# Kernel optimization log

Hardware: AMD Instinct MI355X
Metric: run time of the kernel (lower is better)

The kernel has to match this reference:

```python
import jax, jax.numpy as jnp
import numpy as np

N = 100000      # nodes
E = 1600000     # edges per direction
G = 512         # graphs in the batch
NEG_SLOPE = 0.2 # PyG GATConv default


def _gat_conv(x, W, a_s, a_d, b, src, dst, n):
    # PyG GATConv, heads=1: h = x W; e_ij = LeakyReLU(a_s.h_j + a_d.h_i);
    # softmax over incoming edges of i; out_i = sum_j alpha_ij h_j + b
    h = x @ W                                   # [N, F]
    al_s = h @ a_s                              # [N]
    al_d = h @ a_d                              # [N]
    e = jax.nn.leaky_relu(al_s[src] + al_d[dst], NEG_SLOPE)   # [E+N]
    m = jax.ops.segment_max(e, dst, num_segments=n)
    ex = jnp.exp(e - m[dst])
    denom = jax.ops.segment_sum(ex, dst, num_segments=n)
    coef = ex / denom[dst]                      # softmax per destination
    out = jax.ops.segment_sum(h[src] * coef[:, None], dst, num_segments=n)
    return out + b


def _branch(x, edge_index, W1, as1, ad1, b1, W2, as2, ad2, b2, batch, n, g):
    # add self loops (GATConv default add_self_loops=True)
    loops = jnp.arange(n)
    src = jnp.concatenate([edge_index[0], loops])
    dst = jnp.concatenate([edge_index[1], loops])
    h = jax.nn.relu(_gat_conv(x, W1, as1, ad1, b1, src, dst, n))
    # dropout is identity at eval time
    h = jax.nn.relu(_gat_conv(h, W2, as2, ad2, b2, src, dst, n))
    s = jax.ops.segment_sum(h, batch, num_segments=g)
    cnt = jax.ops.segment_sum(jnp.ones((n,), h.dtype), batch, num_segments=g)
    return s / jnp.maximum(cnt, 1.0)[:, None]    # scatter_mean


def setup_inputs() -> dict:
    key = jax.random.key(0)
    ks = jax.random.split(key, 24)
    d_in, d_hid, d_out, n_cls = 128, 128, 128, 4
    x = jax.random.normal(ks[0], (N, d_in), jnp.float32)
    td = jax.random.randint(ks[1], (2, E), 0, N)
    bu = jax.random.randint(ks[2], (2, E), 0, N)
    batch = jnp.sort(jax.random.randint(ks[3], (N,), 0, G))

    def lin(k, shape):
        return jax.random.normal(k, shape, jnp.float32) * (1.0 / np.sqrt(shape[0]))

    inp = {"x": x, "td_edge_index": td, "bu_edge_index": bu, "batch": batch}
    i = 4
    for br in ("td", "bu"):
        for layer, (di, do) in (("1", (d_in, d_hid)), ("2", (d_hid, d_out))):
            inp[f"{br}_W{layer}"] = lin(ks[i], (di, do)); i += 1
            inp[f"{br}_as{layer}"] = lin(ks[i], (do,)); i += 1
            inp[f"{br}_ad{layer}"] = lin(ks[i], (do,)); i += 1
            inp[f"{br}_b{layer}"] = jnp.zeros((do,), jnp.float32)
    inp["fc_W"] = lin(ks[i], (2 * d_out, n_cls)); i += 1
    inp["fc_b"] = jnp.zeros((n_cls,), jnp.float32)
    return inp


def reference(x, td_edge_index, bu_edge_index, batch,
              td_W1, td_as1, td_ad1, td_b1, td_W2, td_as2, td_ad2, td_b2,
              bu_W1, bu_as1, bu_ad1, bu_b1, bu_W2, bu_as2, bu_ad2, bu_b2,
              fc_W, fc_b):
    td = _branch(x, td_edge_index, td_W1, td_as1, td_ad1, td_b1,
                 td_W2, td_as2, td_ad2, td_b2, batch, N, G)
    bu = _branch(x, bu_edge_index, bu_W1, bu_as1, bu_ad1, bu_b1,
                 bu_W2, bu_as2, bu_ad2, bu_b2, batch, N, G)
    out = jnp.concatenate([bu, td], axis=1) @ fc_W + fc_b   # [G, num_class]
    return jax.nn.log_softmax(out, axis=1)
```

## Files before the change

kernel.cpp:

```cpp
#include <hip/hip_runtime.h>

#define FD 128
#define SB 512
#define CHK 8192

typedef __attribute__((ext_vector_type(8))) short bf16x8;
typedef __attribute__((ext_vector_type(4))) float f32x4;

static inline size_t roundup256(size_t x) { return (x + 255) & ~(size_t)255; }

__device__ __forceinline__ unsigned short f2bf(float f) {
    unsigned u = __float_as_uint(f);
    u += 0x7FFFu + ((u >> 16) & 1u);
    return (unsigned short)(u >> 16);
}
__device__ __forceinline__ float bflo(unsigned v) { return __uint_as_float(v << 16); }
__device__ __forceinline__ float bfhi(unsigned v) { return __uint_as_float(v & 0xFFFF0000u); }

__global__ __launch_bounds__(256) void wprep_kernel(
    const float* __restrict__ w0, const float* __restrict__ w1,
    const float* __restrict__ w2, const float* __restrict__ w3,
    unsigned short* __restrict__ out)
{
    const int widx = blockIdx.x >> 6;
    const float* src = (widx == 0) ? w0 : (widx == 1) ? w1 : (widx == 2) ? w2 : w3;
    const int flat = (blockIdx.x & 63) * 256 + threadIdx.x;
    const int k = flat >> 7, n = flat & 127;
    const int dest = ((((n >> 4) * 4 + (k >> 5)) * 4 + ((k >> 3) & 3)) * 16 + (n & 15)) * 8 + (k & 7);
    out[widx * 16384 + dest] = f2bf(src[flat]);
}

__global__ __launch_bounds__(256) void bucket_count_kernel(
    const int* __restrict__ td_ei, const int* __restrict__ bu_ei,
    int* __restrict__ table, int E, int NB, int NBLK)
{
    __shared__ int cnt[512];
    const int blk = blockIdx.x;
    const int br = blk / NBLK, c = blk % NBLK;
    const int* edst = (br ? bu_ei : td_ei) + E;
    for (int i = threadIdx.x; i < NB; i += 256) cnt[i] = 0;
    __syncthreads();
    const int k0 = c * CHK;
    #pragma unroll 4
    for (int j = 0; j < CHK / 256; ++j) {
        const int k = k0 + j * 256 + threadIdx.x;
        if (k < E) atomicAdd(&cnt[((unsigned)edst[k]) >> 8], 1);
    }
    __syncthreads();
    for (int i = threadIdx.x; i < NB; i += 256)
        table[(br * NB + i) * NBLK + c] = cnt[i];
}

__global__ __launch_bounds__(256) void bucket_scatter_kernel(
    const int* __restrict__ td_ei, const int* __restrict__ bu_ei,
    const int* __restrict__ scanned, int* __restrict__ bucketed,
    int E, int NB, int NBLK)
{
    __shared__ int cur[512];
    const int blk = blockIdx.x;
    const int br = blk / NBLK, c = blk % NBLK;
    const int* ei = br ? bu_ei : td_ei;
    for (int i = threadIdx.x; i < NB; i += 256)
        cur[i] = scanned[(br * NB + i) * NBLK + c];
    __syncthreads();
    const int k0 = c * CHK;
    #pragma unroll 4
    for (int j = 0; j < CHK / 256; ++j) {
        const int k = k0 + j * 256 + threadIdx.x;
        if (k < E) {
            const int d = ei[E + k], s = ei[k];
            const int pos = atomicAdd(&cur[((unsigned)d) >> 8], 1);
            bucketed[pos] = ((d & 255) << 24) | s;
        }
    }
}

__global__ __launch_bounds__(256) void bucket_finalize_kernel(
    const int* __restrict__ scanned, const int* __restrict__ bucketed,
    int* __restrict__ esorted, int* __restrict__ rowptr,
    int E, int N, int NB, int NBLK)
{
    __shared__ int bins[256], off[256], curs[256], tmp[256];
    const int gb = blockIdx.x;
    const int br = gb / NB, lb = gb % NB;
    const int tid = threadIdx.x;
    const int base = scanned[gb * NBLK];
    const int next = scanned[(gb + 1) * NBLK];
    const int s = next - base;

    bins[tid] = 0;
    __syncthreads();
    for (int i = base + tid; i < base + s; i += 256)
        atomicAdd(&bins[((unsigned)bucketed[i]) >> 24], 1);
    __syncthreads();
    const int v = bins[tid];
    tmp[tid] = v;
    __syncthreads();
    for (int o = 1; o < 256; o <<= 1) {
        const int t = (tid >= o) ? tmp[tid - o] : 0;
        __syncthreads();
        tmp[tid] += t;
        __syncthreads();
    }
    off[tid] = tmp[tid] - v;
    curs[tid] = tmp[tid] - v;
    const int nd = N - lb * 256;
    if (tid < nd && tid < 256) rowptr[br * N + lb * 256 + tid] = base + off[tid];
    if (gb == 2 * NB - 1 && tid == 0) rowptr[2 * N] = 2 * E;
    __syncthreads();
    for (int i = base + tid; i < base + s; i += 256) {
        const int p = bucketed[i];
        const int r = atomicAdd(&curs[((unsigned)p) >> 24], 1);
        esorted[base + r] = br * N + (p & 0xFFFFFF);
    }
}

__global__ __launch_bounds__(SB) void scan_block_kernel(
    const int* __restrict__ in, int* __restrict__ out, int* __restrict__ bsum, int n)
{
    __shared__ int sh[SB];
    const int tid = threadIdx.x;
    const int i = blockIdx.x * SB + tid;
    int v = (i < n) ? in[i] : 0;
    sh[tid] = v;
    __syncthreads();
    for (int off = 1; off < SB; off <<= 1) {
        int t = (tid >= off) ? sh[tid - off] : 0;
        __syncthreads();
        sh[tid] += t;
        __syncthreads();
    }
    if (i < n) out[i] = sh[tid] - v;
    if (tid == SB - 1) bsum[blockIdx.x] = sh[tid];
}

__global__ __launch_bounds__(SB) void scan_top_kernel(int* __restrict__ bsum, int nb)
{
    __shared__ int sh[SB];
    const int tid = threadIdx.x;
    int v = (tid < nb) ? bsum[tid] : 0;
    sh[tid] = v;
    __syncthreads();
    for (int off = 1; off < SB; off <<= 1) {
        int t = (tid >= off) ? sh[tid - off] : 0;
        __syncthreads();
        sh[tid] += t;
        __syncthreads();
    }
    if (tid < nb) bsum[tid] = sh[tid] - v;
}

__global__ __launch_bounds__(SB) void scan_add_kernel(
    int* __restrict__ arr, const int* __restrict__ bsum, int n, int total)
{
    int i = blockIdx.x * SB + threadIdx.x;
    if (i < n) arr[i] += bsum[blockIdx.x];
    if (i == 0) arr[n] = total;
}

template<bool A_F32>
__global__ __launch_bounds__(256) void gemm_mfma_kernel(
    const float* __restrict__ Xf, const unsigned short* __restrict__ Xb,
    const unsigned short* __restrict__ Wfrag,
    const float* __restrict__ as0, const float* __restrict__ ad0,
    const float* __restrict__ as1, const float* __restrict__ ad1,
    unsigned short* __restrict__ H16, float* __restrict__ als, float* __restrict__ ald,
    int nrows, int xbstride)
{
    const int tid = threadIdx.x;
    const int br  = blockIdx.y;
    const int w = tid >> 6, l = tid & 63, lg = l >> 4, cl = l & 15;
    const int lr0 = blockIdx.x * 64 + w * 16;
    const int lr  = lr0 + cl;
    const unsigned short* Wb = Wfrag + br * 16384;
    const float* a_s = br ? as1 : as0;
    const float* a_d = br ? ad1 : ad0;

    bf16x8 a[4];
    if (lr < nrows) {
        if (A_F32) {
            const float* xp = Xf + (size_t)(br * xbstride + lr) * FD + lg * 8;
            #pragma unroll
            for (int ks = 0; ks < 4; ++ks) {
                const float4 v0 = *(const float4*)(xp + ks * 32);
                const float4 v1 = *(const float4*)(xp + ks * 32 + 4);
                bf16x8 t;
                t[0] = (short)f2bf(v0.x); t[1] = (short)f2bf(v0.y);
                t[2] = (short)f2bf(v0.z); t[3] = (short)f2bf(v0.w);
                t[4] = (short)f2bf(v1.x); t[5] = (short)f2bf(v1.y);
                t[6] = (short)f2bf(v1.z); t[7] = (short)f2bf(v1.w);
                a[ks] = t;
            }
        } else {
            const unsigned short* xp = Xb + (size_t)(br * xbstride + lr) * FD + lg * 8;
            #pragma unroll
            for (int ks = 0; ks < 4; ++ks) a[ks] = *(const bf16x8*)(xp + ks * 32);
        }
    } else {
        #pragma unroll
        for (int ks = 0; ks < 4; ++ks)
            #pragma unroll
            for (int j = 0; j < 8; ++j) a[ks][j] = 0;
    }

    f32x4 acc[8];
    #pragma unroll
    for (int t = 0; t < 8; ++t)
        #pragma unroll
        for (int j = 0; j < 4; ++j) acc[t][j] = 0.f;

    #pragma unroll
    for (int t = 0; t < 8; ++t) {
        #pragma unroll
        for (int ks = 0; ks < 4; ++ks) {
            const bf16x8 b = *(const bf16x8*)&Wb[(((t * 4 + ks) * 4 + lg) * 16 + cl) * 8];
            acc[t] = __builtin_amdgcn_mfma_f32_16x16x32_bf16(a[ks], b, acc[t], 0, 0, 0);
        }
    }

    float asv[8], adv[8];
    #pragma unroll
    for (int t = 0; t < 8; ++t) { asv[t] = a_s[t * 16 + cl]; adv[t] = a_d[t * 16 + cl]; }

    #pragma unroll
    for (int jj = 0; jj < 4; ++jj) {
        const int lrow = lr0 + 4 * lg + jj;
        float ps = 0.f, pd = 0.f;
        #pragma unroll
        for (int t = 0; t < 8; ++t) {
            ps = fmaf(acc[t][jj], asv[t], ps);
            pd = fmaf(acc[t][jj], adv[t], pd);
        }
        #pragma unroll
        for (int off = 8; off; off >>= 1) {
            ps += __shfl_down(ps, off, 16);
            pd += __shfl_down(pd, off, 16);
        }
        if (lrow < nrows) {
            const size_t grow = (size_t)br * nrows + lrow;
            #pragma unroll
            for (int t = 0; t < 8; ++t)
                H16[grow * FD + t * 16 + cl] = f2bf(acc[t][jj]);
            if (cl == 0) { als[grow] = ps; ald[grow] = pd; }
        }
    }
}

__global__ __launch_bounds__(256) void gat_aggregate_kernel(
    const int* __restrict__ rowptr, const int* __restrict__ esorted,
    const float* __restrict__ als, const float* __restrict__ ald,
    const unsigned short* __restrict__ H16,
    const float* __restrict__ b0, const float* __restrict__ b1,
    unsigned short* __restrict__ out16, int n2, int N)
{
    const int d    = (int)((blockIdx.x * 256u + threadIdx.x) >> 5);
    const int lane = threadIdx.x & 31;
    if (d >= n2) return;
    const int start = rowptr[d], end = rowptr[d + 1];
    const int deg = end - start;
    const float ald_d = ald[d];
    const int c = lane * 4;
    const float* bias = (d < N) ? b0 : b1;

    const uint2 hs = *(const uint2*)&H16[(size_t)d * FD + c];

    float e_self = als[d] + ald_d;
    e_self = fmaxf(e_self, 0.2f * e_self);

    float e_reg = -INFINITY;
    int src_reg = 0;
    if (lane < deg) {
        src_reg = esorted[start + lane];
        float t = als[src_reg] + ald_d;
        e_reg = fmaxf(t, 0.2f * t);
    }
    float m = e_reg;
    for (int j = start + 32 + lane; j < end; j += 32) {
        float t = als[esorted[j]] + ald_d;
        m = fmaxf(m, fmaxf(t, 0.2f * t));
    }
    #pragma unroll
    for (int off = 16; off; off >>= 1) m = fmaxf(m, __shfl_xor(m, off, 32));
    m = fmaxf(m, e_self);

    const float w_self = __expf(e_self - m);
    const float w_reg  = __expf(e_reg - m);

    float dsum = w_reg;
    #pragma unroll
    for (int off = 16; off; off >>= 1) dsum += __shfl_xor(dsum, off, 32);
    float denom = dsum + w_self;

    float a0 = w_self * bflo(hs.x);
    float a1 = w_self * bfhi(hs.x);
    float a2 = w_self * bflo(hs.y);
    float a3 = w_self * bfhi(hs.y);

    const int dmin = deg < 32 ? deg : 32;
    int j = 0;
    for (; j + 7 < dmin; j += 8) {
        uint2 hv[8];
        float w[8];
        #pragma unroll
        for (int q = 0; q < 8; ++q) {
            const int s = __shfl(src_reg, j + q, 32);
            w[q] = __shfl(w_reg, j + q, 32);
            hv[q] = *(const uint2*)&H16[(size_t)s * FD + c];
        }
        #pragma unroll
        for (int q = 0; q < 8; ++q) {
            a0 = fmaf(w[q], bflo(hv[q].x), a0);
            a1 = fmaf(w[q], bfhi(hv[q].x), a1);
            a2 = fmaf(w[q], bflo(hv[q].y), a2);
            a3 = fmaf(w[q], bfhi(hv[q].y), a3);
        }
    }
    for (; j < dmin; ++j) {
        const int   s = __shfl(src_reg, j, 32);
        const float w = __shfl(w_reg, j, 32);
        const uint2 hv = *(const uint2*)&H16[(size_t)s * FD + c];
        a0 = fmaf(w, bflo(hv.x), a0);
        a1 = fmaf(w, bfhi(hv.x), a1);
        a2 = fmaf(w, bflo(hv.y), a2);
        a3 = fmaf(w, bfhi(hv.y), a3);
    }
    for (int jj = 32; jj < deg; ++jj) {
        const int s = esorted[start + jj];
        float t = als[s] + ald_d;
        t = fmaxf(t, 0.2f * t);
        const float w = __expf(t - m);
        denom += w;
        const uint2 hv = *(const uint2*)&H16[(size_t)s * FD + c];
        a0 = fmaf(w, bflo(hv.x), a0);
        a1 = fmaf(w, bfhi(hv.x), a1);
        a2 = fmaf(w, bflo(hv.y), a2);
        a3 = fmaf(w, bfhi(hv.y), a3);
    }
    const float inv = 1.f / denom;
    const float4 bb = *(const float4*)&bias[c];
    const float o0 = fmaxf(fmaf(a0, inv, bb.x), 0.f);
    const float o1 = fmaxf(fmaf(a1, inv, bb.y), 0.f);
    const float o2 = fmaxf(fmaf(a2, inv, bb.z), 0.f);
    const float o3 = fmaxf(fmaf(a3, inv, bb.w), 0.f);
    uint2 ov;
    ov.x = (unsigned)f2bf(o0) | ((unsigned)f2bf(o1) << 16);
    ov.y = (unsigned)f2bf(o2) | ((unsigned)f2bf(o3) << 16);
    *(uint2*)&out16[(size_t)d * FD + c] = ov;
}

__global__ __launch_bounds__(256) void pool_mean_kernel(
    const unsigned short* __restrict__ Hb, const int* __restrict__ batch,
    float* __restrict__ pooled_td, float* __restrict__ pooled_bu, int n)
{
    __shared__ float sh[3][FD];
    const int g = blockIdx.x;
    const int br = blockIdx.y;
    int lo = 0, hi = n;
    while (lo < hi) { int mid = (lo + hi) >> 1; if (batch[mid] < g) lo = mid + 1; else hi = mid; }
    int start = lo;
    hi = n;
    while (lo < hi) { int mid = (lo + hi) >> 1; if (batch[mid] < g + 1) lo = mid + 1; else hi = mid; }
    int end = lo;
    const int cp = threadIdx.x & 63;
    const int q  = threadIdx.x >> 6;
    const size_t rbase = (size_t)br * n;
    float ax = 0.f, ay = 0.f;
    for (int i = start + q; i < end; i += 4) {
        unsigned v = ((const unsigned*)Hb)[(rbase + i) * 64 + cp];
        ax += bflo(v);
        ay += bfhi(v);
    }
    if (q) { sh[q - 1][cp * 2] = ax; sh[q - 1][cp * 2 + 1] = ay; }
    __syncthreads();
    if (!q) {
        float tx = ax + sh[0][cp * 2] + sh[1][cp * 2] + sh[2][cp * 2];
        float ty = ay + sh[0][cp * 2 + 1] + sh[1][cp * 2 + 1] + sh[2][cp * 2 + 1];
        float inv = 1.f / fmaxf((float)(end - start), 1.f);
        float* out = br ? pooled_bu : pooled_td;
        out[(size_t)g * FD + cp * 2]     = tx * inv;
        out[(size_t)g * FD + cp * 2 + 1] = ty * inv;
    }
}

__global__ __launch_bounds__(256) void fc_logsoftmax_kernel(
    const float* __restrict__ bu, const float* __restrict__ td,
    const float* __restrict__ Wf, const float* __restrict__ bf,
    float* __restrict__ out, int g)
{
    const int wid  = (int)((blockIdx.x * 256u + threadIdx.x) >> 6);
    const int lane = threadIdx.x & 63;
    if (wid >= g) return;
    const float f0 = bu[(size_t)wid * FD + lane];
    const float f1 = bu[(size_t)wid * FD + 64 + lane];
    const float f2 = td[(size_t)wid * FD + lane];
    const float f3 = td[(size_t)wid * FD + 64 + lane];
    const float4 w0 = *(const float4*)&Wf[lane * 4];
    const float4 w1 = *(const float4*)&Wf[(64 + lane) * 4];
    const float4 w2 = *(const float4*)&Wf[(128 + lane) * 4];
    const float4 w3 = *(const float4*)&Wf[(192 + lane) * 4];
    float l0 = f0 * w0.x + f1 * w1.x + f2 * w2.x + f3 * w3.x;
    float l1 = f0 * w0.y + f1 * w1.y + f2 * w2.y + f3 * w3.y;
    float l2 = f0 * w0.z + f1 * w1.z + f2 * w2.z + f3 * w3.z;
    float l3 = f0 * w0.w + f1 * w1.w + f2 * w2.w + f3 * w3.w;
    #pragma unroll
    for (int off = 32; off; off >>= 1) {
        l0 += __shfl_xor(l0, off, 64);
        l1 += __shfl_xor(l1, off, 64);
        l2 += __shfl_xor(l2, off, 64);
        l3 += __shfl_xor(l3, off, 64);
    }
    if (lane == 0) {
        l0 += bf[0]; l1 += bf[1]; l2 += bf[2]; l3 += bf[3];
        float m = fmaxf(fmaxf(l0, l1), fmaxf(l2, l3));
        float ssum = expf(l0 - m) + expf(l1 - m) + expf(l2 - m) + expf(l3 - m);
        float ls = logf(ssum);
        out[(size_t)wid * 4 + 0] = l0 - m - ls;
        out[(size_t)wid * 4 + 1] = l1 - m - ls;
        out[(size_t)wid * 4 + 2] = l2 - m - ls;
        out[(size_t)wid * 4 + 3] = l3 - m - ls;
    }
}

extern "C" void kernel_launch(void* const* d_in, const int* in_sizes, int n_in,
                              void* d_out, int out_size, void* d_ws, size_t ws_size,
                              hipStream_t stream)
{
    const float* x      = (const float*)d_in[0];
    const int*   td_ei  = (const int*)d_in[1];
    const int*   bu_ei  = (const int*)d_in[2];
    const int*   batch  = (const int*)d_in[3];
    const float* td_W1  = (const float*)d_in[4];
    const float* td_as1 = (const float*)d_in[5];
    const float* td_ad1 = (const float*)d_in[6];
    const float* td_b1  = (const float*)d_in[7];
    const float* td_W2  = (const float*)d_in[8];
    const float* td_as2 = (const float*)d_in[9];
    const float* td_ad2 = (const float*)d_in[10];
    const float* td_b2  = (const float*)d_in[11];
    const float* bu_W1  = (const float*)d_in[12];
    const float* bu_as1 = (const float*)d_in[13];
    const float* bu_ad1 = (const float*)d_in[14];
    const float* bu_b1  = (const float*)d_in[15];
    const float* bu_W2  = (const float*)d_in[16];
    const float* bu_as2 = (const float*)d_in[17];
    const float* bu_ad2 = (const float*)d_in[18];
    const float* bu_b2  = (const float*)d_in[19];
    const float* fc_W   = (const float*)d_in[20];
    const float* fc_b   = (const float*)d_in[21];

    const int N  = in_sizes[0] / FD;
    const int E  = in_sizes[1] / 2;
    const int G  = out_size / 4;
    const int N2 = 2 * N;
    const int NB   = (N + 255) / 256;
    const int NBLK = (E + CHK - 1) / CHK;
    const int TN   = 2 * NB * NBLK;
    const int tnb  = (TN + SB - 1) / SB;
    const int gx   = (N + 63) / 64;

    char* p = (char*)d_ws;
    unsigned short* h16 = (unsigned short*)p; p += roundup256((size_t)N2 * FD * 2);
    unsigned short* o16 = (unsigned short*)p; p += roundup256((size_t)N2 * FD * 2);
    int* esorted  = (int*)p; p += roundup256((size_t)2 * E * 4);
    int* bucketed = (int*)p; p += roundup256((size_t)2 * E * 4);
    int* table    = (int*)p; p += roundup256((size_t)(TN + 1) * 4);
    float* als  = (float*)p;  p += roundup256((size_t)N2 * 4);
    float* ald  = (float*)p;  p += roundup256((size_t)N2 * 4);
    int* rowptr = (int*)p;    p += roundup256((size_t)(N2 + 1) * 4);
    int* bsum   = (int*)p;    p += roundup256((size_t)SB * 4);
    unsigned short* wfrag = (unsigned short*)p; p += roundup256((size_t)4 * 16384 * 2);
    float* pooled_td = (float*)p; p += roundup256((size_t)G * FD * 4);
    float* pooled_bu = (float*)p; p += roundup256((size_t)G * FD * 4);

    const dim3 blk256(256);
    const dim3 gGemm(gx, 2);
    const dim3 gAgg(((unsigned)N2 * 32 + 255) / 256);

    wprep_kernel<<<dim3(256), blk256, 0, stream>>>(td_W1, bu_W1, td_W2, bu_W2, wfrag);

    bucket_count_kernel<<<dim3(2 * NBLK), blk256, 0, stream>>>(td_ei, bu_ei, table, E, NB, NBLK);
    scan_block_kernel<<<dim3(tnb), dim3(SB), 0, stream>>>(table, table, bsum, TN);
    scan_top_kernel<<<dim3(1), dim3(SB), 0, stream>>>(bsum, tnb);
    scan_add_kernel<<<dim3(tnb), dim3(SB), 0, stream>>>(table, bsum, TN, 2 * E);
    bucket_scatter_kernel<<<dim3(2 * NBLK), blk256, 0, stream>>>(td_ei, bu_ei, table, bucketed, E, NB, NBLK);
    bucket_finalize_kernel<<<dim3(2 * NB), blk256, 0, stream>>>(table, bucketed, esorted, rowptr, E, N, NB, NBLK);

    gemm_mfma_kernel<true><<<gGemm, blk256, 0, stream>>>(
        x, (const unsigned short*)nullptr, wfrag,
        td_as1, td_ad1, bu_as1, bu_ad1, h16, als, ald, N, 0);
    gat_aggregate_kernel<<<gAgg, blk256, 0, stream>>>(
        rowptr, esorted, als, ald, h16, td_b1, bu_b1, o16, N2, N);

    gemm_mfma_kernel<false><<<gGemm, blk256, 0, stream>>>(
        (const float*)nullptr, o16, wfrag + 2 * 16384,
        td_as2, td_ad2, bu_as2, bu_ad2, h16, als, ald, N, N);
    gat_aggregate_kernel<<<gAgg, blk256, 0, stream>>>(
        rowptr, esorted, als, ald, h16, td_b2, bu_b2, o16, N2, N);

    pool_mean_kernel<<<dim3(G, 2), blk256, 0, stream>>>(o16, batch, pooled_td, pooled_bu, N);
    fc_logsoftmax_kernel<<<dim3((G + 3) / 4), blk256, 0, stream>>>(
        pooled_bu, pooled_td, fc_W, fc_b, (float*)d_out, G);
}
```

Before: 418.6 us.

## Fuse layer-1 GAT aggregation with layer-2 MFMA GEMM in one kernel

Layer-1 softmax aggregation now writes each block's 16 destination rows into shared memory as bf16 MFMA fragments, and the same block then runs the layer-2 projection and attention-logit reductions. This removes the round trip of the intermediate activation through global memory and drops one kernel launch. Ping-pong buffers and separate als2/ald2 arrays avoid overwriting the inputs still being read. In exchange, blocks of 16 rows must first synchronise on the slowest (highest-degree) node before the GEMM stage, and each block needs a full 128x128 weight read for only 16 rows.

```diff
diff --git a/kernel.cpp b/kernel.cpp
--- a/kernel.cpp
+++ b/kernel.cpp
@@ -158,14 +158,12 @@
     if (i == 0) arr[n] = total;
 }
 
-template<bool A_F32>
-__global__ __launch_bounds__(256) void gemm_mfma_kernel(
-    const float* __restrict__ Xf, const unsigned short* __restrict__ Xb,
-    const unsigned short* __restrict__ Wfrag,
+__global__ __launch_bounds__(256) void gemm_l1_kernel(
+    const float* __restrict__ Xf, const unsigned short* __restrict__ Wfrag,
     const float* __restrict__ as0, const float* __restrict__ ad0,
     const float* __restrict__ as1, const float* __restrict__ ad1,
     unsigned short* __restrict__ H16, float* __restrict__ als, float* __restrict__ ald,
-    int nrows, int xbstride)
+    int nrows)
 {
     const int tid = threadIdx.x;
     const int br  = blockIdx.y;
@@ -178,23 +176,17 @@
 
     bf16x8 a[4];
     if (lr < nrows) {
-        if (A_F32) {
-            const float* xp = Xf + (size_t)(br * xbstride + lr) * FD + lg * 8;
-            #pragma unroll
-            for (int ks = 0; ks < 4; ++ks) {
-                const float4 v0 = *(const float4*)(xp + ks * 32);
-                const float4 v1 = *(const float4*)(xp + ks * 32 + 4);
-                bf16x8 t;
-                t[0] = (short)f2bf(v0.x); t[1] = (short)f2bf(v0.y);
-                t[2] = (short)f2bf(v0.z); t[3] = (short)f2bf(v0.w);
-                t[4] = (short)f2bf(v1.x); t[5] = (short)f2bf(v1.y);
-                t[6] = (short)f2bf(v1.z); t[7] = (short)f2bf(v1.w);
-                a[ks] = t;
-            }
-        } else {
-            const unsigned short* xp = Xb + (size_t)(br * xbstride + lr) * FD + lg * 8;
-            #pragma unroll
-            for (int ks = 0; ks < 4; ++ks) a[ks] = *(const bf16x8*)(xp + ks * 32);
+        const float* xp = Xf + (size_t)lr * FD + lg * 8;
+        #pragma unroll
+        for (int ks = 0; ks < 4; ++ks) {
+            const float4 v0 = *(const float4*)(xp + ks * 32);
+            const float4 v1 = *(const float4*)(xp + ks * 32 + 4);
+            bf16x8 t;
+            t[0] = (short)f2bf(v0.x); t[1] = (short)f2bf(v0.y);
+            t[2] = (short)f2bf(v0.z); t[3] = (short)f2bf(v0.w);
+            t[4] = (short)f2bf(v1.x); t[5] = (short)f2bf(v1.y);
+            t[6] = (short)f2bf(v1.z); t[7] = (short)f2bf(v1.w);
+            a[ks] = t;
         }
     } else {
         #pragma unroll
@@ -346,6 +338,173 @@
     ov.x = (unsigned)f2bf(o0) | ((unsigned)f2bf(o1) << 16);
     ov.y = (unsigned)f2bf(o2) | ((unsigned)f2bf(o3) << 16);
     *(uint2*)&out16[(size_t)d * FD + c] = ov;
+}
+
+__global__ __launch_bounds__(512) void fused_agg_gemm_kernel(
+    const int* __restrict__ rowptr, const int* __restrict__ esorted,
+    const float* __restrict__ als, const float* __restrict__ ald,
+    const unsigned short* __restrict__ H16,
+    const float* __restrict__ b0, const float* __restrict__ b1,
+    const unsigned short* __restrict__ wfrag2,
+    const float* __restrict__ as_td, const float* __restrict__ ad_td,
+    const float* __restrict__ as_bu, const float* __restrict__ ad_bu,
+    unsigned short* __restrict__ H2,
+    float* __restrict__ als2, float* __restrict__ ald2,
+    int n2, int N)
+{
+    __shared__ unsigned short Afrag[4][4][16][8];
+    __shared__ float alsp[16][8], aldp[16][8];
+
+    const int tid  = threadIdx.x;
+    const int hw   = tid >> 5;
+    const int lane = tid & 31;
+    const int d0   = blockIdx.x * 16;
+    const int d    = d0 + hw;
+    const int c    = lane * 4;
+    const int ksw  = c >> 5, lgw = (c >> 3) & 3, jw = c & 7;
+
+    if (d < n2) {
+        const int start = rowptr[d], end = rowptr[d + 1];
+        const int deg = end - start;
+        const float ald_d = ald[d];
+        const float* bias = (d < N) ? b0 : b1;
+
+        const uint2 hs = *(const uint2*)&H16[(size_t)d * FD + c];
+
+        float e_self = als[d] + ald_d;
+        e_self = fmaxf(e_self, 0.2f * e_self);
+
+        float e_reg = -INFINITY;
+        int src_reg = 0;
+        if (lane < deg) {
+            src_reg = esorted[start + lane];
+            float t = als[src_reg] + ald_d;
+            e_reg = fmaxf(t, 0.2f * t);
+        }
+        float m = e_reg;
+        for (int j = start + 32 + lane; j < end; j += 32) {
+            float t = als[esorted[j]] + ald_d;
+            m = fmaxf(m, fmaxf(t, 0.2f * t));
+        }
+        #pragma unroll
+        for (int off = 16; off; off >>= 1) m = fmaxf(m, __shfl_xor(m, off, 32));
+        m = fmaxf(m, e_self);
+
+        const float w_self = __expf(e_self - m);
+        const float w_reg  = __expf(e_reg - m);
+
+        float dsum = w_reg;
+        #pragma unroll
+        for (int off = 16; off; off >>= 1) dsum += __shfl_xor(dsum, off, 32);
+        float denom = dsum + w_self;
+
+        float a0 = w_self * bflo(hs.x);
+        float a1 = w_self * bfhi(hs.x);
+        float a2 = w_self * bflo(hs.y);
+        float a3 = w_self * bfhi(hs.y);
+
+        const int dmin = deg < 32 ? deg : 32;
+        int j = 0;
+        for (; j + 7 < dmin; j += 8) {
+            uint2 hv[8];
+            float w[8];
+            #pragma unroll
+            for (int q = 0; q < 8; ++q) {
+                const int s = __shfl(src_reg, j + q, 32);
+                w[q] = __shfl(w_reg, j + q, 32);
+                hv[q] = *(const uint2*)&H16[(size_t)s * FD + c];
+            }
+            #pragma unroll
+            for (int q = 0; q < 8; ++q) {
+                a0 = fmaf(w[q], bflo(hv[q].x), a0);
+                a1 = fmaf(w[q], bfhi(hv[q].x), a1);
+                a2 = fmaf(w[q], bflo(hv[q].y), a2);
+                a3 = fmaf(w[q], bfhi(hv[q].y), a3);
+            }
+        }
+        for (; j < dmin; ++j) {
+            const int   s = __shfl(src_reg, j, 32);
+            const float w = __shfl(w_reg, j, 32);
+            const uint2 hv = *(const uint2*)&H16[(size_t)s * FD + c];
+            a0 = fmaf(w, bflo(hv.x), a0);
+            a1 = fmaf(w, bfhi(hv.x), a1);
+            a2 = fmaf(w, bflo(hv.y), a2);
+            a3 = fmaf(w, bfhi(hv.y), a3);
+        }
+        for (int jj = 32; jj < deg; ++jj) {
+            const int s = esorted[start + jj];
+            float t = als[s] + ald_d;
+            t = fmaxf(t, 0.2f * t);
+            const float w = __expf(t - m);
+            denom += w;
+            const uint2 hv = *(const uint2*)&H16[(size_t)s * FD + c];
+            a0 = fmaf(w, bflo(hv.x), a0);
+            a1 = fmaf(w, bfhi(hv.x), a1);
+            a2 = fmaf(w, bflo(hv.y), a2);
+            a3 = fmaf(w, bfhi(hv.y), a3);
+        }
+        const float inv = 1.f / denom;
+        const float4 bb = *(const float4*)&bias[c];
+        const float o0 = fmaxf(fmaf(a0, inv, bb.x), 0.f);
+        const float o1 = fmaxf(fmaf(a1, inv, bb.y), 0.f);
+        const float o2 = fmaxf(fmaf(a2, inv, bb.z), 0.f);
+        const float o3 = fmaxf(fmaf(a3, inv, bb.w), 0.f);
+        uint2 pk;
+        pk.x = (unsigned)f2bf(o0) | ((unsigned)f2bf(o1) << 16);
+        pk.y = (unsigned)f2bf(o2) | ((unsigned)f2bf(o3) << 16);
+        *(uint2*)&Afrag[ksw][lgw][hw][jw] = pk;
+    } else {
+        *(uint2*)&Afrag[ksw][lgw][hw][jw] = make_uint2(0u, 0u);
+    }
+    __syncthreads();
+
+    const int w   = tid >> 6;
+    const int l   = tid & 63;
+    const int lg2 = l >> 4, cl = l & 15;
+    const int br  = (d0 >= N) ? 1 : 0;
+    const unsigned short* Wb = wfrag2 + br * 16384;
+    const float* a_s = br ? as_bu : as_td;
+    const float* a_d = br ? ad_bu : ad_td;
+
+    bf16x8 a[4];
+    #pragma unroll
+    for (int ks = 0; ks < 4; ++ks)
+        a[ks] = *(const bf16x8*)&Afrag[ks][lg2][cl][0];
+
+    f32x4 acc = {0.f, 0.f, 0.f, 0.f};
+    #pragma unroll
+    for (int ks = 0; ks < 4; ++ks) {
+        const bf16x8 b = *(const bf16x8*)&Wb[(((w * 4 + ks) * 4 + lg2) * 16 + cl) * 8];
+        acc = __builtin_amdgcn_mfma_f32_16x16x32_bf16(a[ks], b, acc, 0, 0, 0);
+    }
+
+    const float asv = a_s[w * 16 + cl];
+    const float adv = a_d[w * 16 + cl];
+    #pragma unroll
+    for (int jj = 0; jj < 4; ++jj) {
+        const int lrow = 4 * lg2 + jj;
+        const int grow = d0 + lrow;
+        if (grow < n2) H2[(size_t)grow * FD + w * 16 + cl] = f2bf(acc[jj]);
+        float t1 = acc[jj] * asv;
+        float t2 = acc[jj] * adv;
+        #pragma unroll
+        for (int off = 8; off; off >>= 1) {
+            t1 += __shfl_down(t1, off, 16);
+            t2 += __shfl_down(t2, off, 16);
+        }
+        if (cl == 0) { alsp[lrow][w] = t1; aldp[lrow][w] = t2; }
+    }
+    __syncthreads();
+    if (tid < 16) {
+        const int grow = d0 + tid;
+        if (grow < n2) {
+            float s = 0.f, dd = 0.f;
+            #pragma unroll
+            for (int q = 0; q < 8; ++q) { s += alsp[tid][q]; dd += aldp[tid][q]; }
+            als2[grow] = s;
+            ald2[grow] = dd;
+        }
+    }
 }
 
 __global__ __launch_bounds__(256) void pool_mean_kernel(
@@ -466,6 +625,8 @@
     int* table    = (int*)p; p += roundup256((size_t)(TN + 1) * 4);
     float* als  = (float*)p;  p += roundup256((size_t)N2 * 4);
     float* ald  = (float*)p;  p += roundup256((size_t)N2 * 4);
+    float* als2 = (float*)p;  p += roundup256((size_t)N2 * 4);
+    float* ald2 = (float*)p;  p += roundup256((size_t)N2 * 4);
     int* rowptr = (int*)p;    p += roundup256((size_t)(N2 + 1) * 4);
     int* bsum   = (int*)p;    p += roundup256((size_t)SB * 4);
     unsigned short* wfrag = (unsigned short*)p; p += roundup256((size_t)4 * 16384 * 2);
@@ -475,6 +636,7 @@
     const dim3 blk256(256);
     const dim3 gGemm(gx, 2);
     const dim3 gAgg(((unsigned)N2 * 32 + 255) / 256);
+    const dim3 gFused((N2 + 15) / 16);
 
     wprep_kernel<<<dim3(256), blk256, 0, stream>>>(td_W1, bu_W1, td_W2, bu_W2, wfrag);
 
@@ -485,19 +647,18 @@
     bucket_scatter_kernel<<<dim3(2 * NBLK), blk256, 0, stream>>>(td_ei, bu_ei, table, bucketed, E, NB, NBLK);
     bucket_finalize_kernel<<<dim3(2 * NB), blk256, 0, stream>>>(table, bucketed, esorted, rowptr, E, N, NB, NBLK);
 
-    gemm_mfma_kernel<true><<<gGemm, blk256, 0, stream>>>(
-        x, (const unsigned short*)nullptr, wfrag,
-        td_as1, td_ad1, bu_as1, bu_ad1, h16, als, ald, N, 0);
+    gemm_l1_kernel<<<gGemm, blk256, 0, stream>>>(
+        x, wfrag, td_as1, td_ad1, bu_as1, bu_ad1, h16, als, ald, N);
+
+    fused_agg_gemm_kernel<<<gFused, dim3(512), 0, stream>>>(
+        rowptr, esorted, als, ald, h16, td_b1, bu_b1,
+        wfrag + 2 * 16384, td_as2, td_ad2, bu_as2, bu_ad2,
+        o16, als2, ald2, N2, N);
+
     gat_aggregate_kernel<<<gAgg, blk256, 0, stream>>>(
-        rowptr, esorted, als, ald, h16, td_b1, bu_b1, o16, N2, N);
-
-    gemm_mfma_kernel<false><<<gGemm, blk256, 0, stream>>>(
-        (const float*)nullptr, o16, wfrag + 2 * 16384,
-        td_as2, td_ad2, bu_as2, bu_ad2, h16, als, ald, N, N);
-    gat_aggregate_kernel<<<gAgg, blk256, 0, stream>>>(
-        rowptr, esorted, als, ald, h16, td_b2, bu_b2, o16, N2, N);
-
-    pool_mean_kernel<<<dim3(G, 2), blk256, 0, stream>>>(o16, batch, pooled_td, pooled_bu, N);
+        rowptr, esorted, als2, ald2, o16, td_b2, bu_b2, h16, N2, N);
+
+    pool_mean_kernel<<<dim3(G, 2), blk256, 0, stream>>>(h16, batch, pooled_td, pooled_bu, N);
     fc_logsoftmax_kernel<<<dim3((G + 3) / 4), blk256, 0, stream>>>(
         pooled_bu, pooled_td, fc_W, fc_b, (float*)d_out, G);
 }
```

Result: slower. 431.5 us (+3.1%).
